# Kernel tuning notes

Hardware: AMD Instinct MI355X
Metric: run time of the kernel (lower is better)

## Reference

```python
import jax, jax.numpy as jnp
import numpy as np

L = 2048         # new tokens (prefill)
HID = 4096
NH = 32          # attention heads
NKV = 8          # kv heads
HD = HID // NH   # 128
MAX = 4096       # kv-cache capacity
EPS = 1e-5


def _rope_tables(L, HD):
    inv_freq = 1.0 / (10000.0 ** (np.arange(0, HD, 2, dtype=np.float32) / HD))
    ang = np.arange(L, dtype=np.float32)[:, None] * inv_freq[None, :]  # [L, HD/2]
    ang = np.concatenate([ang, ang], axis=-1)                          # HF duplicated layout
    return jnp.asarray(np.cos(ang)), jnp.asarray(np.sin(ang))


def setup_inputs() -> dict:
    key = jax.random.key(0)
    ks = jax.random.split(key, 6)
    cos, sin = _rope_tables(L, HD)
    s = 0.02
    return {
        "x": jax.random.normal(ks[0], (L, HID), jnp.float32),
        "cos": cos,
        "sin": sin,
        "position_ids": jnp.arange(L, dtype=jnp.int64),
        "seq_len": L,
        "k_cache": jnp.zeros((MAX, NKV, HD), jnp.float32),
        "v_cache": jnp.zeros((MAX, NKV, HD), jnp.float32),
        "ln_w": jnp.ones((HID,), jnp.float32),
        "Wq": jax.random.normal(ks[1], (NH * HD, HID), jnp.float32) * s,
        "Wk": jax.random.normal(ks[2], (NKV * HD, HID), jnp.float32) * s,
        "Wv": jax.random.normal(ks[3], (NKV * HD, HID), jnp.float32) * s,
        "Wo": jax.random.normal(ks[4], (HID, NH * HD), jnp.float32) * s,
    }


def _rms_norm(x, w, eps=EPS):
    xf = x.astype(jnp.float32)
    var = jnp.mean(xf * xf, axis=-1, keepdims=True)
    return (w * (xf * jax.lax.rsqrt(var + eps))).astype(x.dtype)


def _rotate_half(x):
    x1, x2 = jnp.split(x, 2, axis=-1)
    return jnp.concatenate([-x2, x1], axis=-1)


def reference(x, cos, sin, position_ids, seq_len, k_cache, v_cache, ln_w, Wq, Wk, Wv, Wo):
    Lq, hid = x.shape
    nkv, hd = k_cache.shape[1], k_cache.shape[2]
    nh = Wq.shape[0] // hd
    g = nh // nkv

    residual = x
    h = _rms_norm(x, ln_w)

    q = (h @ Wq.T).reshape(Lq, nh, hd)
    k = (h @ Wk.T).reshape(Lq, nkv, hd)
    v = (h @ Wv.T).reshape(Lq, nkv, hd)

    # RoPE, cos/sin broadcast over heads (unsqueeze_dim=1)
    c = cos[:, None, :]
    s = sin[:, None, :]
    q = q * c + _rotate_half(q) * s
    k = k * c + _rotate_half(k) * s

    # KV-cache scatter write
    k_cache = k_cache.at[position_ids].set(k)
    v_cache = v_cache.at[position_ids].set(v)

    # prefill path (num_new_tokens > 1): causal GQA SDPA over new keys only
    scale = 1.0 / jnp.sqrt(jnp.asarray(hd, jnp.float32))
    qg = q.reshape(Lq, nkv, g, hd)
    scores = jnp.einsum('qhgd,khd->hgqk', qg, k) * scale  # [nkv, g, Lq, Lq]
    idx = jnp.arange(Lq)
    causal = idx[None, :] <= idx[:, None]                  # [Lq, Lq]
    scores = jnp.where(causal[None, None], scores, -jnp.inf)
    p = jax.nn.softmax(scores, axis=-1)
    attn = jnp.einsum('hgqk,khd->qhgd', p, v).reshape(Lq, nh * hd)

    out = residual + attn @ Wo.T
    return out, k_cache, v_cache
```

## Files before the change

kernel.cpp:

```cpp
#include <hip/hip_runtime.h>
#include <hip/hip_bf16.h>
#include <cstdint>

#define L_SEQ 2048
#define HID   4096
#define NH    32
#define NKV   8
#define HD    128
#define MAXP  4096
#define QKVD  6144
#define K_OFF 4096
#define V_OFF 5120

using bf16_t = __hip_bfloat16;
typedef __bf16 bf16x8 __attribute__((ext_vector_type(8)));
typedef float  f32x4  __attribute__((ext_vector_type(4)));
typedef short  short4v __attribute__((ext_vector_type(4)));
typedef short  short8v __attribute__((ext_vector_type(8)));

__device__ __forceinline__ void async_copy16(void* lds, const void* g) {
  __builtin_amdgcn_global_load_lds(
      (__attribute__((address_space(1))) void*)g,
      (__attribute__((address_space(3))) void*)lds, 16, 0, 0);
}

__device__ __forceinline__ f32x4 MFMA16(bf16x8 a, bf16x8 b, f32x4 c) {
  return __builtin_amdgcn_mfma_f32_16x16x32_bf16(a, b, c, 0, 0, 0);
}

__global__ __launch_bounds__(256) void rmsnorm_kernel(
    const float* __restrict__ x, const float* __restrict__ w,
    bf16_t* __restrict__ h) {
  int row = blockIdx.x, t = threadIdx.x;
  const float4* xv = (const float4*)(x + (size_t)row * HID);
  float4 v[4];
  float ss = 0.f;
#pragma unroll
  for (int i = 0; i < 4; i++) {
    v[i] = xv[i * 256 + t];
    ss += v[i].x * v[i].x + v[i].y * v[i].y + v[i].z * v[i].z + v[i].w * v[i].w;
  }
#pragma unroll
  for (int off = 32; off >= 1; off >>= 1) ss += __shfl_xor(ss, off, 64);
  __shared__ float red[4];
  if ((t & 63) == 0) red[t >> 6] = ss;
  __syncthreads();
  float rr = rsqrtf((red[0] + red[1] + red[2] + red[3]) * (1.0f / HID) + 1e-5f);
  const float4* wv = (const float4*)w;
  bf16_t* hr = h + (size_t)row * HID;
#pragma unroll
  for (int i = 0; i < 4; i++) {
    float4 wl = wv[i * 256 + t];
    bf16_t tmp[4];
    tmp[0] = __float2bfloat16(v[i].x * rr * wl.x);
    tmp[1] = __float2bfloat16(v[i].y * rr * wl.y);
    tmp[2] = __float2bfloat16(v[i].z * rr * wl.z);
    tmp[3] = __float2bfloat16(v[i].w * rr * wl.w);
    *(short4v*)(hr + (size_t)(i * 256 + t) * 4) = *(short4v*)tmp;
  }
}

__global__ __launch_bounds__(256) void cvt_bf16_kernel(
    const float* __restrict__ src, bf16_t* __restrict__ dst) {
  size_t i = ((size_t)blockIdx.x * 256 + threadIdx.x) * 8;
  float4 a = *(const float4*)(src + i);
  float4 b = *(const float4*)(src + i + 4);
  bf16_t tmp[8] = {__float2bfloat16(a.x), __float2bfloat16(a.y),
                   __float2bfloat16(a.z), __float2bfloat16(a.w),
                   __float2bfloat16(b.x), __float2bfloat16(b.y),
                   __float2bfloat16(b.z), __float2bfloat16(b.w)};
  *(short8v*)(dst + i) = *(short8v*)tmp;
}

#define STR2_(x) #x
#define STR_(x) STR2_(x)

template <int OUT_MODE>
__global__ __launch_bounds__(512, 2) void gemm256_kernel(
    const bf16_t* __restrict__ A, const bf16_t* __restrict__ B,
    bf16_t* __restrict__ Cb, float* __restrict__ Cf,
    const float* __restrict__ resid, int N, int K) {
  __shared__ alignas(16) bf16_t As[2 * 2 * 8192];
  __shared__ alignas(16) bf16_t Bs[2 * 2 * 8192];

  const int t = threadIdx.x;
  const int l = t & 63;
  const int w = t >> 6;
  const int wm = w >> 2;
  const int wn = w & 3;
  const int wh = wn >> 1;
  const int wn1 = wn & 1;
  const int lane15 = l & 15, quad = l >> 4;
  const int l7 = l & 7;

  const bf16_t* Ag = A + (size_t)blockIdx.y * 256 * K;
  const bf16_t* Bg = B + (size_t)blockIdx.x * 256 * K;

  const int srow = t >> 3;
  const int sgran = (t & 7) ^ (srow & 7);
  const int wbase = w << 9;

  const bf16_t* pAg = Ag + (size_t)srow * K + sgran * 8;
  const bf16_t* pBg = Bg + (size_t)srow * K + sgran * 8;
  const size_t row64 = (size_t)64 * K;

#define STAGE(PL, UOFF, ldsh) do {                                            \
    const bf16_t* _g = (PL) + (UOFF);                                         \
    async_copy16((ldsh) + wbase, _g);                                         \
    async_copy16((ldsh) + wbase + 4096, _g + row64);                          \
  } while (0)

#define ASD(sl, h) (&As[(sl) * 16384 + (h) * 8192])
#define BSD(sl, h) (&Bs[(sl) * 16384 + (h) * 8192])

  typedef __attribute__((address_space(3))) char* lds_b;
  lds_b asb = (lds_b)As;
  lds_b bsb = (lds_b)Bs;
  const unsigned aoff0 = (unsigned)(wm * 16384 + lane15 * 128 + ((quad ^ l7) << 4));
  const unsigned boff0 = (unsigned)(wh * 16384 + (wn1 * 64 + lane15) * 128 + ((quad ^ l7) << 4));
  lds_b pa0s0 = asb + aoff0;
  lds_b pa1s0 = asb + (aoff0 ^ 64u);
  lds_b pa0s1 = pa0s0 + 32768;
  lds_b pa1s1 = pa1s0 + 32768;
  lds_b pb0s0 = bsb + boff0;
  lds_b pb1s0 = bsb + (boff0 ^ 64u);
  lds_b pb0s1 = pb0s0 + 32768;
  lds_b pb1s1 = pb1s0 + 32768;

#define DSR(dst, p, IMM) \
  asm volatile("ds_read_b128 %0, %1 offset:" STR_(IMM) : "=v"(dst) : "v"(p))

#define RA(dst, P0, P1, I0, I1, I2, I3) do {                                  \
    DSR(dst[0][0], P0, I0); DSR(dst[0][1], P1, I0);                           \
    DSR(dst[1][0], P0, I1); DSR(dst[1][1], P1, I1);                           \
    DSR(dst[2][0], P0, I2); DSR(dst[2][1], P1, I2);                           \
    DSR(dst[3][0], P0, I3); DSR(dst[3][1], P1, I3); } while (0)
#define RB(dst, P0, P1, I0, I1) do {                                          \
    DSR(dst[0][0], P0, I0); DSR(dst[0][1], P1, I0);                           \
    DSR(dst[1][0], P0, I1); DSR(dst[1][1], P1, I1); } while (0)

#define BAR() do { asm volatile("s_barrier");                                 \
    __builtin_amdgcn_sched_barrier(0); } while (0)
#define LGKM(NW) do { asm volatile("s_waitcnt lgkmcnt(" STR_(NW) ")");        \
    __builtin_amdgcn_sched_barrier(0); } while (0)
#define VMW(NW) asm volatile("s_waitcnt vmcnt(" STR_(NW) ")")

#define MMQ(IB, JB, AF, BF) do {                                              \
    __builtin_amdgcn_s_setprio(1);                                            \
    _Pragma("unroll") for (int i = 0; i < 4; i++)                             \
    _Pragma("unroll") for (int j = 0; j < 2; j++) {                           \
      acc[(IB)+i][(JB)+j] = MFMA16(AF[i][0], BF[j][0], acc[(IB)+i][(JB)+j]);  \
      acc[(IB)+i][(JB)+j] = MFMA16(AF[i][1], BF[j][1], acc[(IB)+i][(JB)+j]);  \
    }                                                                         \
    __builtin_amdgcn_s_setprio(0);                                            \
    __builtin_amdgcn_sched_barrier(0);                                        \
  } while (0)

  const size_t u128 = (size_t)128 * K;
  const int NTT = K >> 6;
  const int niter = NTT >> 1;

  f32x4 acc[8][4] = {};
  bf16x8 a[4][2], a2[4][2], blo[2][2], bhi[2][2];

  STAGE(pBg, 0,          BSD(0, 0));
  STAGE(pAg, 0,          ASD(0, 0));
  STAGE(pBg, u128,       BSD(0, 1));
  STAGE(pAg, u128,       ASD(0, 1));
  STAGE(pBg, 64,         BSD(1, 0));
  STAGE(pAg, 64,         ASD(1, 0));
  VMW(4);
  BAR();
  RA(a, pa0s0, pa1s0, 0, 2048, 4096, 6144);
  RB(blo, pb0s0, pb1s0, 0, 2048);

  for (int it = 0; it < niter; ++it) {
    const int tb = it * 2;
    const size_t kc1 = (size_t)((tb + 1) << 6);
    const size_t kc2 = (size_t)(((tb + 2 < NTT) ? tb + 2 : NTT - 1) << 6);
    const size_t kc3 = (size_t)(((tb + 3 < NTT) ? tb + 3 : NTT - 1) << 6);
    STAGE(pBg, u128 + kc1, BSD(1, 1));
    BAR();
    RB(bhi, pb0s0, pb1s0, 4096, 6144);
    LGKM(4);
    MMQ(0, 0, a, blo);
    BAR();
    STAGE(pAg, u128 + kc1, ASD(1, 1));
    BAR();
    RA(a2, pa0s0, pa1s0, 8192, 10240, 12288, 14336);
    LGKM(8);
    MMQ(0, 2, a, bhi);
    BAR();
    STAGE(pBg, kc2, BSD(0, 0));
    BAR();
    LGKM(0);
    MMQ(4, 0, a2, blo);
    BAR();
    STAGE(pAg, kc2, ASD(0, 0));
    VMW(4);
    BAR();
    RA(a, pa0s1, pa1s1, 0, 2048, 4096, 6144);
    RB(blo, pb0s1, pb1s1, 0, 2048);
    LGKM(12);
    MMQ(4, 2, a2, bhi);
    BAR();
    STAGE(pBg, u128 + kc2, BSD(0, 1));
    BAR();
    RB(bhi, pb0s1, pb1s1, 4096, 6144);
    LGKM(4);
    MMQ(0, 0, a, blo);
    BAR();
    STAGE(pAg, u128 + kc2, ASD(0, 1));
    BAR();
    RA(a2, pa0s1, pa1s1, 8192, 10240, 12288, 14336);
    LGKM(8);
    MMQ(0, 2, a, bhi);
    BAR();
    STAGE(pBg, kc3, BSD(1, 0));
    BAR();
    LGKM(0);
    MMQ(4, 0, a2, blo);
    BAR();
    STAGE(pAg, kc3, ASD(1, 0));
    VMW(4);
    BAR();
    if (it + 1 < niter) {
      RA(a, pa0s0, pa1s0, 0, 2048, 4096, 6144);
      RB(blo, pb0s0, pb1s0, 0, 2048);
    }
    LGKM(12);
    MMQ(4, 2, a2, bhi);
    BAR();
  }
  VMW(0);

  const int row0 = blockIdx.y * 256 + wm * 128 + quad * 4;
  const int col0 = blockIdx.x * 256 + wn * 64 + lane15;
#pragma unroll
  for (int i = 0; i < 8; i++)
#pragma unroll
    for (int j = 0; j < 4; j++)
#pragma unroll
      for (int r = 0; r < 4; r++) {
        size_t idx = (size_t)(row0 + i * 16 + r) * N + col0 + j * 16;
        if (OUT_MODE == 0)
          Cb[idx] = __float2bfloat16(acc[i][j][r]);
        else
          Cf[idx] = acc[i][j][r] + resid[idx];
      }
#undef STAGE
#undef ASD
#undef BSD
#undef DSR
#undef RA
#undef RB
#undef BAR
#undef LGKM
#undef VMW
#undef MMQ
}

__global__ __launch_bounds__(256) void rope_kernel(
    bf16_t* __restrict__ qkv,
    const float* __restrict__ cosT, const float* __restrict__ sinT,
    float* __restrict__ kc_out) {
  int idx = blockIdx.x * 256 + threadIdx.x;
  int d = idx & 63;
  int rest = idx >> 6;
  int hh = rest % (NH + NKV);
  int pos = rest / (NH + NKV);
  float c = cosT[pos * HD + d];
  float s = sinT[pos * HD + d];
  bf16_t* b = (hh < NH)
      ? qkv + (size_t)pos * QKVD + hh * HD
      : qkv + (size_t)pos * QKVD + K_OFF + (hh - NH) * HD;
  float x1 = __bfloat162float(b[d]);
  float x2 = __bfloat162float(b[d + 64]);
  float o1 = x1 * c - x2 * s;
  float o2 = x2 * c + x1 * s;
  b[d] = __float2bfloat16(o1);
  b[d + 64] = __float2bfloat16(o2);
  if (hh >= NH) {
    float* kc = kc_out + (size_t)pos * (NKV * HD) + (hh - NH) * HD;
    kc[d] = o1;
    kc[d + 64] = o2;
  }
}

__global__ __launch_bounds__(256) void vtrans_kernel(
    const bf16_t* __restrict__ qkv, float* __restrict__ vc_out,
    bf16_t* __restrict__ vT) {
  __shared__ alignas(16) short Ts[64 * 64];
  int kvh = blockIdx.x, pb = blockIdx.y, db = blockIdx.z;
  int t = threadIdx.x;
  int r = t & 63;
  int c4 = t >> 6;
  const short* src = (const short*)(qkv + (size_t)(pb * 64 + r) * QKVD +
                                    V_OFF + kvh * HD + db * 64 + c4 * 16);
  short8v v0 = *(const short8v*)src;
  short8v v1 = *(const short8v*)(src + 8);
  float* vo = vc_out + (size_t)(pb * 64 + r) * (NKV * HD) + kvh * HD + db * 64 + c4 * 16;
  float tmpf[16];
#pragma unroll
  for (int j = 0; j < 8; j++) {
    tmpf[j]     = __uint_as_float(((unsigned)(unsigned short)v0[j]) << 16);
    tmpf[j + 8] = __uint_as_float(((unsigned)(unsigned short)v1[j]) << 16);
  }
#pragma unroll
  for (int j = 0; j < 4; j++)
    ((float4*)vo)[j] = make_float4(tmpf[j * 4], tmpf[j * 4 + 1],
                                   tmpf[j * 4 + 2], tmpf[j * 4 + 3]);
  int cs = c4 ^ (r & 3);
  *(short8v*)&Ts[r * 64 + cs * 16] = v0;
  *(short8v*)&Ts[r * 64 + cs * 16 + 8] = v1;
  __syncthreads();
  int dr = t & 63;
  int pc = t >> 6;
  short vals[16];
#pragma unroll
  for (int j = 0; j < 16; j++) {
    int pos = pc * 16 + j;
    int cc = (dr >> 4) ^ (pos & 3);
    vals[j] = Ts[pos * 64 + cc * 16 + (dr & 15)];
  }
  short* dst = (short*)(vT + ((size_t)kvh * HD + db * 64 + dr) * L_SEQ + pb * 64 + pc * 16);
  *(short8v*)dst = *(short8v*)&vals[0];
  *(short8v*)(dst + 8) = *(short8v*)&vals[8];
}

__global__ __launch_bounds__(256) void cache_tail_kernel(
    const float* __restrict__ kc_in, const float* __restrict__ vc_in,
    float* __restrict__ kc_out, float* __restrict__ vc_out) {
  size_t base = (size_t)L_SEQ * NKV * HD;
  size_t i = base + ((size_t)blockIdx.x * 256 + threadIdx.x) * 4;
  *(float4*)(kc_out + i) = *(const float4*)(kc_in + i);
  *(float4*)(vc_out + i) = *(const float4*)(vc_in + i);
}

__global__ __launch_bounds__(256) void attn_kernel(
    const bf16_t* __restrict__ qkv, const bf16_t* __restrict__ vT,
    bf16_t* __restrict__ attn) {
  int h = blockIdx.x;
  int kvh = h >> 2;
  int t = threadIdx.x, w = t >> 6, l = t & 63;
  int lane15 = l & 15, quad = l >> 4;

  __shared__ alignas(16) bf16_t Ks[2][16 * 512];
  __shared__ alignas(16) bf16_t Vs[2][16 * 512];
  __shared__ alignas(16) bf16_t Ps[4][32 * 68];

  const float scale = 0.08838834764831845f;

#define STAGEATTN(KB, BUF) do {                                               \
    _Pragma("unroll") for (int kk_ = 0; kk_ < 4; kk_++)                       \
      async_copy16(&Ks[BUF][(w * 4 + kk_) * 512],                             \
                   qkv + (size_t)((KB) * 64 + w * 16 + lane15) * QKVD +       \
                       K_OFF + kvh * HD + kk_ * 32 + quad * 8);               \
    _Pragma("unroll") for (int j_ = 0; j_ < 4; j_++) {                        \
      int tt_ = w * 2 + (j_ >> 1), kt_ = j_ & 1;                              \
      async_copy16(&Vs[BUF][(tt_ * 2 + kt_) * 512],                           \
                   vT + ((size_t)kvh * HD + tt_ * 16 + lane15) * L_SEQ +      \
                       (KB) * 64 + kt_ * 32 + quad * 8);                      \
    }                                                                         \
  } while (0)

  for (int sel = 0; sel < 2; ++sel) {
    const int qblk = sel ? 15 - (int)blockIdx.y : (int)blockIdx.y;

    bf16x8 aq[2][4];
#pragma unroll
    for (int i = 0; i < 2; i++)
#pragma unroll
      for (int kk = 0; kk < 4; kk++)
        aq[i][kk] = *(const bf16x8*)(qkv +
            (size_t)(qblk * 128 + w * 32 + i * 16 + lane15) * QKVD +
            h * HD + kk * 32 + quad * 8);

    f32x4 o[2][8] = {};
    float lsum[2][4] = {};
    int rowmax_w = qblk * 128 + w * 32 + 31;
    int nk = 2 * qblk + 2;

    STAGEATTN(0, 0);
    for (int kblk = 0; kblk < nk; kblk++) {
      const int cur = kblk & 1;
      if (kblk + 1 < nk) {
        STAGEATTN(kblk + 1, cur ^ 1);
        asm volatile("s_waitcnt vmcnt(8)");
      } else {
        asm volatile("s_waitcnt vmcnt(0)");
      }
      __builtin_amdgcn_s_barrier();
      __builtin_amdgcn_sched_barrier(0);

      if (kblk * 64 <= rowmax_w) {
        f32x4 sacc[2][4] = {};
        __builtin_amdgcn_s_setprio(1);
#pragma unroll
        for (int n = 0; n < 4; n++)
#pragma unroll
          for (int kk = 0; kk < 4; kk++) {
            bf16x8 b = *(const bf16x8*)&Ks[cur][(n * 4 + kk) * 512 + l * 8];
            sacc[0][n] = MFMA16(aq[0][kk], b, sacc[0][n]);
            sacc[1][n] = MFMA16(aq[1][kk], b, sacc[1][n]);
          }
        __builtin_amdgcn_s_setprio(0);
        bool maskblk = (kblk >= 2 * qblk);
#pragma unroll
        for (int i = 0; i < 2; i++)
#pragma unroll
          for (int n = 0; n < 4; n++) {
            int col = kblk * 64 + n * 16 + lane15;
#pragma unroll
            for (int r = 0; r < 4; r++) {
              float p = __expf(sacc[i][n][r] * scale);
              if (maskblk && col > (qblk * 128 + w * 32 + i * 16 + quad * 4 + r)) p = 0.f;
              lsum[i][r] += p;
              Ps[w][(i * 16 + quad * 4 + r) * 68 + n * 16 + lane15] = __float2bfloat16(p);
            }
          }
        __builtin_amdgcn_s_setprio(1);
#pragma unroll
        for (int i = 0; i < 2; i++)
#pragma unroll
          for (int kt2 = 0; kt2 < 2; kt2++) {
            bf16x8 ap = *(const bf16x8*)&Ps[w][(i * 16 + lane15) * 68 + kt2 * 32 + quad * 8];
#pragma unroll
            for (int tt = 0; tt < 8; tt++) {
              bf16x8 b = *(const bf16x8*)&Vs[cur][(tt * 2 + kt2) * 512 + l * 8];
              o[i][tt] = MFMA16(ap, b, o[i][tt]);
            }
          }
        __builtin_amdgcn_s_setprio(0);
      }
      __builtin_amdgcn_s_barrier();
    }

    float inv[2][4];
#pragma unroll
    for (int i = 0; i < 2; i++)
#pragma unroll
      for (int r = 0; r < 4; r++) {
        float s = lsum[i][r];
#pragma unroll
        for (int off = 1; off < 16; off <<= 1) s += __shfl_xor(s, off, 64);
        inv[i][r] = 1.f / s;
      }
    int qrow0 = qblk * 128 + w * 32;
#pragma unroll
    for (int i = 0; i < 2; i++)
#pragma unroll
      for (int tt = 0; tt < 8; tt++) {
        int col = h * HD + tt * 16 + lane15;
#pragma unroll
        for (int r = 0; r < 4; r++)
          attn[(size_t)(qrow0 + i * 16 + quad * 4 + r) * HID + col] =
              __float2bfloat16(o[i][tt][r] * inv[i][r]);
      }
  }
#undef STAGEATTN
}

extern "C" void kernel_launch(void* const* d_in, const int* in_sizes, int n_in,
                              void* d_out, int out_size, void* d_ws, size_t ws_size,
                              hipStream_t stream) {
  const float* x    = (const float*)d_in[0];
  const float* cosT = (const float*)d_in[1];
  const float* sinT = (const float*)d_in[2];
  const float* kc_in = (const float*)d_in[5];
  const float* vc_in = (const float*)d_in[6];
  const float* ln_w  = (const float*)d_in[7];
  const float* Wq = (const float*)d_in[8];
  const float* Wk = (const float*)d_in[9];
  const float* Wv = (const float*)d_in[10];
  const float* Wo = (const float*)d_in[11];

  float* out    = (float*)d_out;
  float* kc_out = out + (size_t)L_SEQ * HID;
  float* vc_out = kc_out + (size_t)MAXP * NKV * HD;

  char* ws = (char*)d_ws;
  bf16_t* h_bf    = (bf16_t*)(ws + 0);
  bf16_t* attn_bf = (bf16_t*)(ws + 0);
  bf16_t* Wqkv_bf = (bf16_t*)(ws + 16777216);
  bf16_t* Wo_bf   = (bf16_t*)(ws + 16777216);
  bf16_t* qkv_bf  = (bf16_t*)(ws + 67108864);
  bf16_t* vT_bf   = (bf16_t*)(ws + 92274688);

  rmsnorm_kernel<<<L_SEQ, 256, 0, stream>>>(x, ln_w, h_bf);
  cvt_bf16_kernel<<<(HID * HID) / (8 * 256), 256, 0, stream>>>(Wq, Wqkv_bf);
  cvt_bf16_kernel<<<(NKV * HD * HID) / (8 * 256), 256, 0, stream>>>(
      Wk, Wqkv_bf + (size_t)K_OFF * HID);
  cvt_bf16_kernel<<<(NKV * HD * HID) / (8 * 256), 256, 0, stream>>>(
      Wv, Wqkv_bf + (size_t)V_OFF * HID);

  gemm256_kernel<0><<<dim3(QKVD / 256, L_SEQ / 256), 512, 0, stream>>>(
      h_bf, Wqkv_bf, qkv_bf, nullptr, nullptr, QKVD, HID);

  rope_kernel<<<(L_SEQ * (NH + NKV) * 64) / 256, 256, 0, stream>>>(
      qkv_bf, cosT, sinT, kc_out);
  vtrans_kernel<<<dim3(NKV, L_SEQ / 64, HD / 64), 256, 0, stream>>>(
      qkv_bf, vc_out, vT_bf);
  cache_tail_kernel<<<((MAXP - L_SEQ) * NKV * HD) / (4 * 256), 256, 0, stream>>>(
      kc_in, vc_in, kc_out, vc_out);

  cvt_bf16_kernel<<<(HID * HID) / (8 * 256), 256, 0, stream>>>(Wo, Wo_bf);

  attn_kernel<<<dim3(NH, 8), 256, 0, stream>>>(qkv_bf, vT_bf, attn_bf);

  gemm256_kernel<1><<<dim3(HID / 256, L_SEQ / 256), 512, 0, stream>>>(
      attn_bf, Wo_bf, nullptr, out, x, HID, HID);
}
```

Before: 579.0 us.

## Halve attention query tile to 64 rows and double grid for more parallelism

```diff
diff --git a/kernel.cpp b/kernel.cpp
--- a/kernel.cpp
+++ b/kernel.cpp
@@ -337,17 +337,18 @@
   *(float4*)(vc_out + i) = *(const float4*)(vc_in + i);
 }
 
-__global__ __launch_bounds__(256) void attn_kernel(
+__global__ __launch_bounds__(256, 2) void attn_kernel(
     const bf16_t* __restrict__ qkv, const bf16_t* __restrict__ vT,
     bf16_t* __restrict__ attn) {
   int h = blockIdx.x;
+  int pb = blockIdx.y;
   int kvh = h >> 2;
   int t = threadIdx.x, w = t >> 6, l = t & 63;
   int lane15 = l & 15, quad = l >> 4;
 
   __shared__ alignas(16) bf16_t Ks[2][16 * 512];
   __shared__ alignas(16) bf16_t Vs[2][16 * 512];
-  __shared__ alignas(16) bf16_t Ps[4][32 * 68];
+  __shared__ alignas(16) bf16_t Ps[4][16 * 68];
 
   const float scale = 0.08838834764831845f;
 
@@ -365,21 +366,18 @@
   } while (0)
 
   for (int sel = 0; sel < 2; ++sel) {
-    const int qblk = sel ? 15 - (int)blockIdx.y : (int)blockIdx.y;
-
-    bf16x8 aq[2][4];
-#pragma unroll
-    for (int i = 0; i < 2; i++)
-#pragma unroll
-      for (int kk = 0; kk < 4; kk++)
-        aq[i][kk] = *(const bf16x8*)(qkv +
-            (size_t)(qblk * 128 + w * 32 + i * 16 + lane15) * QKVD +
-            h * HD + kk * 32 + quad * 8);
-
-    f32x4 o[2][8] = {};
-    float lsum[2][4] = {};
-    int rowmax_w = qblk * 128 + w * 32 + 31;
-    int nk = 2 * qblk + 2;
+    const int qb = sel ? 31 - pb : pb;
+
+    bf16x8 aq[4];
+#pragma unroll
+    for (int kk = 0; kk < 4; kk++)
+      aq[kk] = *(const bf16x8*)(qkv +
+          (size_t)(qb * 64 + w * 16 + lane15) * QKVD +
+          h * HD + kk * 32 + quad * 8);
+
+    f32x4 o[8] = {};
+    float lsum[4] = {};
+    const int nk = qb + 1;
 
     STAGEATTN(0, 0);
     for (int kblk = 0; kblk < nk; kblk++) {
@@ -393,70 +391,61 @@
       __builtin_amdgcn_s_barrier();
       __builtin_amdgcn_sched_barrier(0);
 
-      if (kblk * 64 <= rowmax_w) {
-        f32x4 sacc[2][4] = {};
-        __builtin_amdgcn_s_setprio(1);
-#pragma unroll
-        for (int n = 0; n < 4; n++)
-#pragma unroll
-          for (int kk = 0; kk < 4; kk++) {
-            bf16x8 b = *(const bf16x8*)&Ks[cur][(n * 4 + kk) * 512 + l * 8];
-            sacc[0][n] = MFMA16(aq[0][kk], b, sacc[0][n]);
-            sacc[1][n] = MFMA16(aq[1][kk], b, sacc[1][n]);
-          }
-        __builtin_amdgcn_s_setprio(0);
-        bool maskblk = (kblk >= 2 * qblk);
-#pragma unroll
-        for (int i = 0; i < 2; i++)
-#pragma unroll
-          for (int n = 0; n < 4; n++) {
-            int col = kblk * 64 + n * 16 + lane15;
-#pragma unroll
-            for (int r = 0; r < 4; r++) {
-              float p = __expf(sacc[i][n][r] * scale);
-              if (maskblk && col > (qblk * 128 + w * 32 + i * 16 + quad * 4 + r)) p = 0.f;
-              lsum[i][r] += p;
-              Ps[w][(i * 16 + quad * 4 + r) * 68 + n * 16 + lane15] = __float2bfloat16(p);
-            }
-          }
-        __builtin_amdgcn_s_setprio(1);
-#pragma unroll
-        for (int i = 0; i < 2; i++)
-#pragma unroll
-          for (int kt2 = 0; kt2 < 2; kt2++) {
-            bf16x8 ap = *(const bf16x8*)&Ps[w][(i * 16 + lane15) * 68 + kt2 * 32 + quad * 8];
-#pragma unroll
-            for (int tt = 0; tt < 8; tt++) {
-              bf16x8 b = *(const bf16x8*)&Vs[cur][(tt * 2 + kt2) * 512 + l * 8];
-              o[i][tt] = MFMA16(ap, b, o[i][tt]);
-            }
-          }
-        __builtin_amdgcn_s_setprio(0);
+      f32x4 sacc[4] = {};
+      __builtin_amdgcn_s_setprio(1);
+#pragma unroll
+      for (int n = 0; n < 4; n++)
+#pragma unroll
+        for (int kk = 0; kk < 4; kk++) {
+          bf16x8 b = *(const bf16x8*)&Ks[cur][(n * 4 + kk) * 512 + l * 8];
+          sacc[n] = MFMA16(aq[kk], b, sacc[n]);
+        }
+      __builtin_amdgcn_s_setprio(0);
+
+      bool maskblk = (kblk == qb);
+#pragma unroll
+      for (int n = 0; n < 4; n++) {
+        int col = kblk * 64 + n * 16 + lane15;
+#pragma unroll
+        for (int r = 0; r < 4; r++) {
+          float p = __expf(sacc[n][r] * scale);
+          if (maskblk && col > (qb * 64 + w * 16 + quad * 4 + r)) p = 0.f;
+          lsum[r] += p;
+          Ps[w][(quad * 4 + r) * 68 + n * 16 + lane15] = __float2bfloat16(p);
+        }
       }
+
+      __builtin_amdgcn_s_setprio(1);
+#pragma unroll
+      for (int kt2 = 0; kt2 < 2; kt2++) {
+        bf16x8 ap = *(const bf16x8*)&Ps[w][lane15 * 68 + kt2 * 32 + quad * 8];
+#pragma unroll
+        for (int tt = 0; tt < 8; tt++) {
+          bf16x8 b = *(const bf16x8*)&Vs[cur][(tt * 2 + kt2) * 512 + l * 8];
+          o[tt] = MFMA16(ap, b, o[tt]);
+        }
+      }
+      __builtin_amdgcn_s_setprio(0);
       __builtin_amdgcn_s_barrier();
     }
 
-    float inv[2][4];
-#pragma unroll
-    for (int i = 0; i < 2; i++)
-#pragma unroll
-      for (int r = 0; r < 4; r++) {
-        float s = lsum[i][r];
-#pragma unroll
-        for (int off = 1; off < 16; off <<= 1) s += __shfl_xor(s, off, 64);
-        inv[i][r] = 1.f / s;
-      }
-    int qrow0 = qblk * 128 + w * 32;
-#pragma unroll
-    for (int i = 0; i < 2; i++)
-#pragma unroll
-      for (int tt = 0; tt < 8; tt++) {
-        int col = h * HD + tt * 16 + lane15;
-#pragma unroll
-        for (int r = 0; r < 4; r++)
-          attn[(size_t)(qrow0 + i * 16 + quad * 4 + r) * HID + col] =
-              __float2bfloat16(o[i][tt][r] * inv[i][r]);
-      }
+    float inv[4];
+#pragma unroll
+    for (int r = 0; r < 4; r++) {
+      float s = lsum[r];
+#pragma unroll
+      for (int off = 1; off < 16; off <<= 1) s += __shfl_xor(s, off, 64);
+      inv[r] = 1.f / s;
+    }
+    int qrow0 = qb * 64 + w * 16;
+#pragma unroll
+    for (int tt = 0; tt < 8; tt++) {
+      int col = h * HD + tt * 16 + lane15;
+#pragma unroll
+      for (int r = 0; r < 4; r++)
+        attn[(size_t)(qrow0 + quad * 4 + r) * HID + col] =
+            __float2bfloat16(o[tt][r] * inv[r]);
+    }
   }
 #undef STAGEATTN
 }
@@ -506,7 +495,7 @@
 
   cvt_bf16_kernel<<<(HID * HID) / (8 * 256), 256, 0, stream>>>(Wo, Wo_bf);
 
-  attn_kernel<<<dim3(NH, 8), 256, 0, stream>>>(qkv_bf, vT_bf, attn_bf);
+  attn_kernel<<<dim3(NH, 16), 256, 0, stream>>>(qkv_bf, vT_bf, attn_bf);
 
   gemm256_kernel<1><<<dim3(HID / 256, L_SEQ / 256), 512, 0, stream>>>(
       attn_bf, Wo_bf, nullptr, out, x, HID, HID);
```

New measurement: 542.7 us. -6.3%, faster.
